# Optimization experiments

Hardware: AMD Instinct MI355X
Metric: run time of the kernel (lower is better)

## Reference

```python
import jax, jax.numpy as jnp
import numpy as np
from jax import lax

NEG = -1e30  # log-space 'zero', fp32-safe
B, T, C, L = 128, 160, 6625, 25


def setup_inputs() -> dict:
    key = jax.random.key(0)
    k1, k2, k3 = jax.random.split(key, 3)
    predicts = jax.random.normal(k1, (B, T, C), dtype=jnp.float32)
    labels = jax.random.randint(k2, (B, L), 1, C, dtype=jnp.int32)  # blank=0 excluded
    label_lengths = jax.random.randint(k3, (B,), 10, L + 1, dtype=jnp.int32)
    return {"predicts": predicts, "labels": labels, "label_lengths": label_lengths}


def _ctc_nll(log_probs, labels, label_lengths):
    # log_probs: [T, B, C] log-softmaxed; labels: [B, L]; lengths: [B]
    Bn, Ln = labels.shape
    S = 2 * Ln + 1  # extended label length (blanks interleaved)
    ext = jnp.zeros((Bn, S), dtype=labels.dtype).at[:, 1::2].set(labels)
    ext_m2 = jnp.pad(ext[:, :-2], ((0, 0), (2, 0)))  # ext shifted by 2 (blank-padded)
    allow_skip = (ext != 0) & (ext != ext_m2) & (jnp.arange(S) >= 2)  # [B, S]

    # gather per-timestep log-probs of extended labels: [T, B, S]
    lp_ext = jnp.take_along_axis(log_probs, ext[None].astype(jnp.int32), axis=2)

    alpha0 = jnp.full((Bn, S), NEG, dtype=log_probs.dtype)
    alpha0 = alpha0.at[:, 0].set(lp_ext[0, :, 0]).at[:, 1].set(lp_ext[0, :, 1])

    def step(alpha, lp_t):
        a1 = jnp.pad(alpha[:, :-1], ((0, 0), (1, 0)), constant_values=NEG)
        a2 = jnp.pad(alpha[:, :-2], ((0, 0), (2, 0)), constant_values=NEG)
        acc = jnp.logaddexp(alpha, a1)
        acc = jnp.where(allow_skip, jnp.logaddexp(acc, a2), acc)
        return acc + lp_t, None

    alphaT, _ = lax.scan(step, alpha0, lp_ext[1:])
    s_last = 2 * label_lengths  # final blank position; s_last-1 = last label
    v_blank = jnp.take_along_axis(alphaT, s_last[:, None], axis=1)[:, 0]
    v_label = jnp.take_along_axis(alphaT, (s_last - 1)[:, None], axis=1)[:, 0]
    return -jnp.logaddexp(v_blank, v_label)  # [B]


def reference(predicts, labels, label_lengths):
    # predicts: [B, T, C] -> permute to [T, B, C], log_softmax over classes
    log_probs = jax.nn.log_softmax(jnp.transpose(predicts, (1, 0, 2)), axis=2)
    loss = _ctc_nll(log_probs, labels, label_lengths)
    # focal reweighting (use_focal_loss=True)
    weight = jnp.square(1.0 - jnp.exp(-loss))
    loss = loss * weight
    return jnp.mean(loss)
```

## Files before the change

kernel.cpp:

```cpp
#include <hip/hip_runtime.h>
#include <cstdint>
#include <cstddef>

#define TT 160
#define BB 128
#define CC 6625
#define LL 25
#define SS 51
#define SP 64
#define NEGV (-1e30f)

__global__ __launch_bounds__(256) void k1_lse_gather(
    const float* __restrict__ pred, const int* __restrict__ labels,
    float* __restrict__ lp_ext, float* __restrict__ out)
{
    const int r = blockIdx.x;
    const int b = r / TT;
    const int t = r - b * TT;
    const float* __restrict__ row = pred + (size_t)r * CC;
    const int tid = threadIdx.x;

    if (r == 0 && tid == 0) out[0] = 0.0f;

    const uintptr_t addr = (uintptr_t)row;
    const int head = (int)(((16u - (unsigned)(addr & 15u)) & 15u) >> 2);
    const int nvec = (CC - head) >> 2;
    const int tail = CC - head - (nvec << 2);
    const float4* __restrict__ vrow = (const float4*)(row + head);

    float4 v[7];
    #pragma unroll
    for (int k = 0; k < 7; ++k) {
        const int j = tid + (k << 8);
        v[k] = (j < nvec) ? vrow[j] : make_float4(NEGV, NEGV, NEGV, NEGV);
    }
    float extra = NEGV;
    if (tid < head)             extra = row[tid];
    else if (tid - head < tail) extra = row[head + (nvec << 2) + (tid - head)];

    float s0 = __expf(extra), s1 = 0.f, s2 = 0.f, s3 = 0.f;
    #pragma unroll
    for (int k = 0; k < 7; ++k) {
        s0 += __expf(v[k].x); s1 += __expf(v[k].y);
        s2 += __expf(v[k].z); s3 += __expf(v[k].w);
    }
    float ssum = (s0 + s1) + (s2 + s3);
    #pragma unroll
    for (int off = 32; off >= 1; off >>= 1) ssum += __shfl_xor(ssum, off, 64);

    __shared__ float sm[4];
    const int lane = tid & 63, wid = tid >> 6;
    if (lane == 0) sm[wid] = ssum;
    __syncthreads();
    const float lse = __logf((sm[0] + sm[1]) + (sm[2] + sm[3]));

    if (tid < SS) {
        const int cls = (tid & 1) ? labels[b * LL + (tid >> 1)] : 0;
        lp_ext[((size_t)b * TT + t) * SP + tid] = row[cls] - lse;
    }
}

__global__ __launch_bounds__(64) void k2_ctc(
    const float* __restrict__ lp_ext, const int* __restrict__ labels,
    const int* __restrict__ lens, float* __restrict__ out)
{
    __shared__ __align__(16) float lp[TT * SP];
    const int b = blockIdx.x;
    const int lane = threadIdx.x;

    const float4* __restrict__ vsrc = (const float4*)(lp_ext + (size_t)b * TT * SP);
    float4* vlds = (float4*)lp;
    #pragma unroll
    for (int rnd = 0; rnd < 5; ++rnd) {
        float4 tmp[8];
        #pragma unroll
        for (int i = 0; i < 8; ++i) tmp[i] = vsrc[lane + 64 * (rnd * 8 + i)];
        #pragma unroll
        for (int i = 0; i < 8; ++i) vlds[lane + 64 * (rnd * 8 + i)] = tmp[i];
    }
    __syncthreads();

    const bool active = (lane < SS);
    int cls = 0, clsm2 = 0;
    if (active && (lane & 1)) {
        cls = labels[b * LL + (lane >> 1)];
        if (lane >= 2) clsm2 = labels[b * LL + ((lane - 2) >> 1)];
    }
    const bool allow = (lane >= 2) && (cls != 0) && (cls != clsm2);

    float alpha = NEGV;
    if (active && lane < 2) alpha = lp[lane];

    for (int t = 1; t < TT; ++t) {
        const float lpv = active ? lp[t * SP + lane] : NEGV;
        float a1 = __shfl_up(alpha, 1, 64);
        float a2 = __shfl_up(alpha, 2, 64);
        if (lane == 0) a1 = NEGV;
        if (lane < 2 || !allow) a2 = NEGV;
        const float m = fmaxf(fmaxf(alpha, a1), a2);
        const float sum = __expf(alpha - m) + __expf(a1 - m) + __expf(a2 - m);
        alpha = m + __logf(sum) + lpv;
    }

    const int sl = 2 * lens[b];
    const float vb = __shfl(alpha, sl, 64);
    const float vl = __shfl(alpha, sl - 1, 64);
    if (lane == 0) {
        const float mm = fmaxf(vb, vl);
        const float loss = -(mm + log1pf(__expf(fminf(vb, vl) - mm)));
        const float w = 1.0f - __expf(-loss);
        atomicAdd(out, loss * w * w * (1.0f / BB));
    }
}

extern "C" void kernel_launch(void* const* d_in, const int* in_sizes, int n_in,
                              void* d_out, int out_size, void* d_ws, size_t ws_size,
                              hipStream_t stream) {
    const float* pred   = (const float*)d_in[0];
    const int*   labels = (const int*)d_in[1];
    const int*   lens   = (const int*)d_in[2];
    float* out    = (float*)d_out;
    float* lp_ext = (float*)d_ws;

    k1_lse_gather<<<BB * TT, 256, 0, stream>>>(pred, labels, lp_ext, out);
    k2_ctc<<<BB, 64, 0, stream>>>(lp_ext, labels, lens, out);
}
```

Before: 706.1 us.

## Process one softmax row per wavefront with nontemporal vector loads

```diff
diff --git a/kernel.cpp b/kernel.cpp
--- a/kernel.cpp
+++ b/kernel.cpp
@@ -10,53 +10,65 @@
 #define SP 64
 #define NEGV (-1e30f)
 
+typedef float v4f __attribute__((ext_vector_type(4)));
+
 __global__ __launch_bounds__(256) void k1_lse_gather(
     const float* __restrict__ pred, const int* __restrict__ labels,
     float* __restrict__ lp_ext, float* __restrict__ out)
 {
-    const int r = blockIdx.x;
+    if (blockIdx.x == 0 && threadIdx.x == 0) out[0] = 0.0f;
+
+    const int wid  = threadIdx.x >> 6;
+    const int lane = threadIdx.x & 63;
+    const int r = blockIdx.x * 4 + wid;
     const int b = r / TT;
     const int t = r - b * TT;
     const float* __restrict__ row = pred + (size_t)r * CC;
-    const int tid = threadIdx.x;
-
-    if (r == 0 && tid == 0) out[0] = 0.0f;
 
     const uintptr_t addr = (uintptr_t)row;
     const int head = (int)(((16u - (unsigned)(addr & 15u)) & 15u) >> 2);
     const int nvec = (CC - head) >> 2;
     const int tail = CC - head - (nvec << 2);
-    const float4* __restrict__ vrow = (const float4*)(row + head);
+    const v4f* __restrict__ vrow = (const v4f*)(row + head);
 
-    float4 v[7];
+    v4f va[9];
     #pragma unroll
-    for (int k = 0; k < 7; ++k) {
-        const int j = tid + (k << 8);
-        v[k] = (j < nvec) ? vrow[j] : make_float4(NEGV, NEGV, NEGV, NEGV);
+    for (int i = 0; i < 9; ++i) va[i] = __builtin_nontemporal_load(&vrow[lane + (i << 6)]);
+    float s0 = 0.f, s1 = 0.f, s2 = 0.f, s3 = 0.f;
+    #pragma unroll
+    for (int i = 0; i < 9; ++i) {
+        s0 += __expf(va[i].x); s1 += __expf(va[i].y);
+        s2 += __expf(va[i].z); s3 += __expf(va[i].w);
     }
+    #pragma unroll
+    for (int i = 0; i < 9; ++i) va[i] = __builtin_nontemporal_load(&vrow[lane + ((i + 9) << 6)]);
+    #pragma unroll
+    for (int i = 0; i < 9; ++i) {
+        s0 += __expf(va[i].x); s1 += __expf(va[i].y);
+        s2 += __expf(va[i].z); s3 += __expf(va[i].w);
+    }
+    #pragma unroll
+    for (int i = 0; i < 7; ++i) va[i] = __builtin_nontemporal_load(&vrow[lane + ((i + 18) << 6)]);
+    va[7] = (1600 + lane < nvec) ? __builtin_nontemporal_load(&vrow[lane + 1600])
+                                 : (v4f){NEGV, NEGV, NEGV, NEGV};
     float extra = NEGV;
-    if (tid < head)             extra = row[tid];
-    else if (tid - head < tail) extra = row[head + (nvec << 2) + (tid - head)];
+    if (lane < head)             extra = row[lane];
+    else if (lane - head < tail) extra = row[head + (nvec << 2) + (lane - head)];
+    s0 += __expf(extra);
+    #pragma unroll
+    for (int i = 0; i < 8; ++i) {
+        s0 += __expf(va[i].x); s1 += __expf(va[i].y);
+        s2 += __expf(va[i].z); s3 += __expf(va[i].w);
+    }
 
-    float s0 = __expf(extra), s1 = 0.f, s2 = 0.f, s3 = 0.f;
-    #pragma unroll
-    for (int k = 0; k < 7; ++k) {
-        s0 += __expf(v[k].x); s1 += __expf(v[k].y);
-        s2 += __expf(v[k].z); s3 += __expf(v[k].w);
-    }
     float ssum = (s0 + s1) + (s2 + s3);
     #pragma unroll
     for (int off = 32; off >= 1; off >>= 1) ssum += __shfl_xor(ssum, off, 64);
+    const float lse = __logf(ssum);
 
-    __shared__ float sm[4];
-    const int lane = tid & 63, wid = tid >> 6;
-    if (lane == 0) sm[wid] = ssum;
-    __syncthreads();
-    const float lse = __logf((sm[0] + sm[1]) + (sm[2] + sm[3]));
-
-    if (tid < SS) {
-        const int cls = (tid & 1) ? labels[b * LL + (tid >> 1)] : 0;
-        lp_ext[((size_t)b * TT + t) * SP + tid] = row[cls] - lse;
+    if (lane < SS) {
+        const int cls = (lane & 1) ? labels[b * LL + (lane >> 1)] : 0;
+        lp_ext[((size_t)b * TT + t) * SP + lane] = row[cls] - lse;
     }
 }
 
@@ -122,6 +134,6 @@
     float* out    = (float*)d_out;
     float* lp_ext = (float*)d_ws;
 
-    k1_lse_gather<<<BB * TT, 256, 0, stream>>>(pred, labels, lp_ext, out);
+    k1_lse_gather<<<(BB * TT) / 4, 256, 0, stream>>>(pred, labels, lp_ext, out);
     k2_ctc<<<BB, 64, 0, stream>>>(lp_ext, labels, lens, out);
 }
```

Result: no change. 707.2 us (+0.2%).
